# Optimization experiments

Hardware: AMD Instinct MI355X
Metric: run time of the kernel (lower is better)

## Reference

```python
import jax, jax.numpy as jnp
import numpy as np

B = 262144   # batch of candidate user-item pairs
D = 256      # concat embedding dim (embedding_dim*8)
H = 128      # hypernet hidden
HD = 32      # expert hidden dim
E = 4        # num experts


def setup_inputs() -> dict:
    key = jax.random.key(0)
    ks = jax.random.split(key, 16)
    def w(k, shape, fan_in):
        return jax.random.normal(k, shape, jnp.float32) * (1.0 / np.sqrt(fan_in))
    return {
        "x": jax.random.normal(ks[0], (B, D), jnp.float32),
        "context_embed": jax.random.normal(ks[1], (D,), jnp.float32),
        # hypernet (soft_module_route)
        "W1": w(ks[2], (D, H), D),   "b1": jnp.zeros((H,), jnp.float32),
        "W2": w(ks[3], (H, H), H),   "b2": jnp.zeros((H,), jnp.float32),
        "W12": w(ks[4], (H, E * E), H), "b12": jnp.zeros((E * E,), jnp.float32),
        "W22": w(ks[5], (H, E), H),     "b22": jnp.zeros((E,), jnp.float32),
        # soft_module experts: stacked per-expert Linear weights
        "Wf1": w(ks[6], (E, D, HD), D), "bf1": jnp.zeros((E, HD), jnp.float32),
        "Wf2": w(ks[7], (E, HD, HD), HD), "bf2": jnp.zeros((E, HD), jnp.float32),
        "Wfin": w(ks[8], (HD, 1), HD),  "bfin": jnp.zeros((1,), jnp.float32),
    }


def reference(x, context_embed, W1, b1, W2, b2, W12, b12, W22, b22,
              Wf1, bf1, Wf2, bf2, Wfin, bfin):
    # hypernet: routing weights from x * context
    embeds = x * context_embed[None, :]                       # [B,D]
    h = jax.nn.relu(embeds @ W1 + b1)                         # [B,H]
    c1 = jax.nn.softmax((h @ W12 + b12).reshape(-1, E, E), axis=1)   # [B,4,4]
    h2 = jax.nn.relu(h @ W2 + b2)                             # [B,H]
    c2 = jax.nn.softmax((h2 @ W22 + b22).reshape(-1, E, 1), axis=1)  # [B,4,1]
    # soft_module: 4 experts per layer, soft combined via c1/c2
    o1 = jax.nn.relu(jnp.einsum('bd,edh->bhe', x, Wf1) + bf1.T)      # [B,HD,E]
    in2 = jnp.einsum('bhe,bef->bhf', o1, c1)                         # [B,HD,E]
    o2 = jax.nn.relu(jnp.einsum('bhe,ehk->bke', in2, Wf2) + bf2.T)   # [B,HD,E]
    in3 = jnp.einsum('bke,bef->bkf', o2, c2)[..., 0]                 # [B,HD]
    return in3 @ Wfin + bfin                                         # [B,1]
```

## Files before the change

kernel.cpp:

```cpp
#include <hip/hip_runtime.h>
#include <hip/hip_bf16.h>

typedef _Float16 f16;
typedef _Float16 half8 __attribute__((ext_vector_type(8)));
typedef _Float16 half4 __attribute__((ext_vector_type(4)));
typedef float floatx4 __attribute__((ext_vector_type(4)));

#define BM 64

#define WA_OFF 0
#define WB_OFF 65536
#define WC_OFF 83968
#define WF2_OFF 86016
#define WSF_BYTE_OFF 180224
#define BA_OFF 0
#define BB_OFF 256
#define BCC_OFF 400
#define BF2_OFF 404
#define WFIN_OFF 532
#define BFIN_OFF 564

__global__ __launch_bounds__(256) void prep_kernel(
    const float* __restrict__ ctx, const float* __restrict__ W1,
    const float* __restrict__ b1, const float* __restrict__ W2,
    const float* __restrict__ b2, const float* __restrict__ W12,
    const float* __restrict__ b12, const float* __restrict__ W22,
    const float* __restrict__ b22, const float* __restrict__ Wf1,
    const float* __restrict__ bf1, const float* __restrict__ Wf2,
    const float* __restrict__ bf2, const float* __restrict__ Wfin,
    const float* __restrict__ bfin, f16* __restrict__ wsh,
    float* __restrict__ wsf)
{
  int tid = blockIdx.x * 256 + threadIdx.x;
  if (tid < 65536) {
    int j = tid & 7, l = (tid >> 3) & 63, kt = (tid >> 9) & 7, nt = tid >> 12;
    int k = kt * 32 + ((l >> 4) << 3) + j, n = nt * 16 + (l & 15);
    float v;
    if (n < 128) v = ctx[k] * W1[k * 128 + n];
    else { int c = n - 128; v = Wf1[((c >> 5) * 256 + k) * 32 + (c & 31)]; }
    wsh[tid] = (f16)v;
  } else if (tid < WB_OFF + 18432) {
    int o = tid - WB_OFF;
    int j = o & 7, l = (o >> 3) & 63, kt = (o >> 9) & 3, nt = o >> 11;
    int k = kt * 32 + ((l >> 4) << 3) + j, n = nt * 16 + (l & 15);
    float v = (n < 128) ? W2[k * 128 + n] : W12[k * 16 + (n - 128)];
    wsh[tid] = (f16)v;
  } else if (tid < WC_OFF + 2048) {
    int o = tid - WC_OFF;
    int j = o & 7, l = (o >> 3) & 63, kt = (o >> 9) & 3;
    int k = kt * 32 + ((l >> 4) << 3) + j, n = l & 15;
    float v = (n < 4) ? W22[k * 4 + n] : 0.f;
    wsh[tid] = (f16)v;
  } else if (tid < WF2_OFF + 4096) {
    int o = tid - WF2_OFF;
    int j = o & 7, l = (o >> 3) & 63, ent = o >> 9;
    int e = ent >> 1, nt = ent & 1;
    int k = ((l >> 4) << 3) + j, n = nt * 16 + (l & 15);
    wsh[tid] = (f16)Wf2[(e * 32 + k) * 32 + n];
  } else if (tid < 90112 + 565) {
    int o = tid - 90112;
    float v;
    if (o < 128) v = b1[o];
    else if (o < 256) v = bf1[o - 128];
    else if (o < 384) v = b2[o - 256];
    else if (o < 400) v = b12[o - 384];
    else if (o < 404) v = b22[o - 400];
    else if (o < 532) v = bf2[o - 404];
    else if (o < 564) v = Wfin[o - 532];
    else v = bfin[0];
    wsf[o] = v;
  }
}

#define MFMA16(A, Bv, C) __builtin_amdgcn_mfma_f32_16x16x32_f16(A, Bv, C, 0, 0, 0)

#define H2_OFF 32768
#define L1_OFF 49152
#define PART_OFF 49152
#define C2_OFF 51200

__global__ __launch_bounds__(512, 3) void fused_kernel(
    const float* __restrict__ x, const f16* __restrict__ wsh,
    const float* __restrict__ wsf, float* __restrict__ out)
{
  __shared__ __attribute__((aligned(16))) char lds[52224];
  const int t = threadIdx.x;
  const int lane = t & 63;
  const int w = t >> 6;
  const int l15 = lane & 15;
  const int l4 = lane >> 4;
  const int sw = (l15 & 7) << 4;
  const size_t base = (size_t)blockIdx.x * BM;

#pragma unroll
  for (int it = 0; it < 4; ++it) {
    int c = it * 512 + t;
    int r = c >> 5;
    int k0 = (c & 31) << 3;
    const float4* xv = (const float4*)(x + (base + (size_t)r) * 256 + k0);
    float4 a = xv[0], b = xv[1];
    half8 hv;
    hv[0] = (f16)a.x; hv[1] = (f16)a.y; hv[2] = (f16)a.z; hv[3] = (f16)a.w;
    hv[4] = (f16)b.x; hv[5] = (f16)b.y; hv[6] = (f16)b.z; hv[7] = (f16)b.w;
    *(half8*)(lds + ((r * 512 + k0 * 2) ^ ((r & 7) << 4))) = hv;
  }
  __syncthreads();

  {
    floatx4 acc[2][4];
#pragma unroll
    for (int q = 0; q < 2; ++q)
#pragma unroll
      for (int mt = 0; mt < 4; ++mt) acc[q][mt] = (floatx4){0.f, 0.f, 0.f, 0.f};
    for (int kt = 0; kt < 8; ++kt) {
      half8 Bx[4];
#pragma unroll
      for (int mt = 0; mt < 4; ++mt) {
        int r = mt * 16 + l15;
        Bx[mt] = *(const half8*)(lds + ((r * 512 + kt * 64 + (l4 << 4)) ^ sw));
      }
#pragma unroll
      for (int q = 0; q < 2; ++q) {
        half8 Wf = *(const half8*)(wsh + WA_OFF + (size_t)(((w * 2 + q) * 8 + kt) * 64 + lane) * 8);
#pragma unroll
        for (int mt = 0; mt < 4; ++mt) acc[q][mt] = MFMA16(Wf, Bx[mt], acc[q][mt]);
      }
    }
    __syncthreads();
#pragma unroll
    for (int q = 0; q < 2; ++q) {
      int c0 = (w * 2 + q) * 16 + l4 * 4;
      float4 bias = *(const float4*)(wsf + BA_OFF + c0);
#pragma unroll
      for (int mt = 0; mt < 4; ++mt) {
        int r = mt * 16 + l15;
        half4 hv;
#pragma unroll
        for (int i = 0; i < 4; ++i) hv[i] = (f16)fmaxf(acc[q][mt][i] + ((const float*)&bias)[i], 0.f);
        *(half4*)(lds + ((r * 512 + c0 * 2) ^ sw)) = hv;
      }
    }
  }
  __syncthreads();

  {
    floatx4 acc2[4];
    floatx4 accL[4];
#pragma unroll
    for (int mt = 0; mt < 4; ++mt) {
      acc2[mt] = (floatx4){0.f, 0.f, 0.f, 0.f};
      accL[mt] = (floatx4){0.f, 0.f, 0.f, 0.f};
    }
    for (int kt = 0; kt < 4; ++kt) {
      half8 Bh[4];
#pragma unroll
      for (int mt = 0; mt < 4; ++mt) {
        int r = mt * 16 + l15;
        Bh[mt] = *(const half8*)(lds + ((r * 512 + kt * 64 + (l4 << 4)) ^ sw));
      }
      half8 Wf = *(const half8*)(wsh + WB_OFF + (size_t)((w * 4 + kt) * 64 + lane) * 8);
#pragma unroll
      for (int mt = 0; mt < 4; ++mt) acc2[mt] = MFMA16(Wf, Bh[mt], acc2[mt]);
      if (w == 7) {
        half8 WfL = *(const half8*)(wsh + WB_OFF + (size_t)((32 + kt) * 64 + lane) * 8);
#pragma unroll
        for (int mt = 0; mt < 4; ++mt) accL[mt] = MFMA16(WfL, Bh[mt], accL[mt]);
      }
    }
    {
      int c0 = w * 16 + l4 * 4;
      float4 bias = *(const float4*)(wsf + BB_OFF + c0);
#pragma unroll
      for (int mt = 0; mt < 4; ++mt) {
        int r = mt * 16 + l15;
        half4 hv;
#pragma unroll
        for (int i = 0; i < 4; ++i) hv[i] = (f16)fmaxf(acc2[mt][i] + ((const float*)&bias)[i], 0.f);
        *(half4*)(lds + H2_OFF + ((r * 256 + c0 * 2) ^ ((r & 7) << 4))) = hv;
      }
    }
    if (w == 7) {
      float4 biasL = *(const float4*)(wsf + BB_OFF + 128 + l4 * 4);
#pragma unroll
      for (int mt = 0; mt < 4; ++mt) {
        int r = mt * 16 + l15;
        half4 hv;
#pragma unroll
        for (int i = 0; i < 4; ++i) hv[i] = (f16)(accL[mt][i] + ((const float*)&biasL)[i]);
        *(half4*)(lds + L1_OFF + r * 32 + l4 * 8) = hv;
      }
    }
  }
  __syncthreads();

  if (w < 4) {
    floatx4 acc3 = (floatx4){0.f, 0.f, 0.f, 0.f};
    int r3 = w * 16 + l15;
#pragma unroll
    for (int kt = 0; kt < 4; ++kt) {
      half8 Bh2 = *(const half8*)(lds + H2_OFF + ((r3 * 256 + kt * 64 + (l4 << 4)) ^ ((r3 & 7) << 4)));
      half8 Wf = *(const half8*)(wsh + WC_OFF + (size_t)(kt * 64 + lane) * 8);
      acc3 = MFMA16(Wf, Bh2, acc3);
    }
    if (lane < 16) {
      float4 bias = *(const float4*)(wsf + BCC_OFF);
      float q0 = acc3[0] + bias.x, q1 = acc3[1] + bias.y;
      float q2 = acc3[2] + bias.z, q3 = acc3[3] + bias.w;
      float m2 = fmaxf(fmaxf(q0, q1), fmaxf(q2, q3));
      float f0 = __expf(q0 - m2), f1 = __expf(q1 - m2);
      float f2 = __expf(q2 - m2), f3 = __expf(q3 - m2);
      float inv2 = 1.f / (f0 + f1 + f2 + f3);
      float4 c2o;
      c2o.x = f0 * inv2; c2o.y = f1 * inv2; c2o.z = f2 * inv2; c2o.w = f3 * inv2;
      *(float4*)(lds + C2_OFF + r3 * 16) = c2o;
    }
  }
  {
    int r = t >> 3, f = (t >> 1) & 3, hh = t & 1;
    const f16* L1p = (const f16*)(lds + L1_OFF) + r * 16 + f;
    float a0 = (float)L1p[0], a1 = (float)L1p[4], a2 = (float)L1p[8], a3 = (float)L1p[12];
    float m = fmaxf(fmaxf(a0, a1), fmaxf(a2, a3));
    float e0 = __expf(a0 - m), e1 = __expf(a1 - m), e2 = __expf(a2 - m), e3 = __expf(a3 - m);
    float inv = 1.f / (e0 + e1 + e2 + e3);
    f16 c0h = (f16)(e0 * inv), c1h = (f16)(e1 * inv);
    f16 c2h = (f16)(e2 * inv), c3h = (f16)(e3 * inv);
    int swr = (r & 7) << 4;
#pragma unroll
    for (int hi = 0; hi < 2; ++hi) {
      int h8 = hh * 2 + hi;
      half8 o0 = *(const half8*)(lds + ((r * 512 + 256 + 0   + h8 * 16) ^ swr));
      half8 o1v = *(const half8*)(lds + ((r * 512 + 256 + 64  + h8 * 16) ^ swr));
      half8 o2v = *(const half8*)(lds + ((r * 512 + 256 + 128 + h8 * 16) ^ swr));
      half8 o3v = *(const half8*)(lds + ((r * 512 + 256 + 192 + h8 * 16) ^ swr));
      half8 res = o0 * c0h + o1v * c1h + o2v * c2h + o3v * c3h;
      *(half8*)(lds + ((r * 512 + f * 64 + h8 * 16) ^ swr)) = res;
    }
  }
  __syncthreads();

  {
    int e = w & 3, ct = w >> 2;
    half8 Wfv = *(const half8*)(wsh + WF2_OFF + (size_t)((e * 2 + ct) * 64 + lane) * 8);
    float4 bv = *(const float4*)(wsf + BF2_OFF + e * 32 + ct * 16 + l4 * 4);
    float4 wfv = *(const float4*)(wsf + WFIN_OFF + ct * 16 + l4 * 4);
    floatx4 a4[4];
#pragma unroll
    for (int mt = 0; mt < 4; ++mt) a4[mt] = (floatx4){0.f, 0.f, 0.f, 0.f};
#pragma unroll
    for (int mt = 0; mt < 4; ++mt) {
      int r = mt * 16 + l15;
      half8 Bi = *(const half8*)(lds + ((r * 512 + e * 64 + (l4 << 4)) ^ ((r & 7) << 4)));
      a4[mt] = MFMA16(Wfv, Bi, a4[mt]);
    }
#pragma unroll
    for (int mt = 0; mt < 4; ++mt) {
      int r = mt * 16 + l15;
      float s = 0.f;
#pragma unroll
      for (int i = 0; i < 4; ++i)
        s += fmaxf(a4[mt][i] + ((const float*)&bv)[i], 0.f) * ((const float*)&wfv)[i];
      s += __shfl_xor(s, 16);
      s += __shfl_xor(s, 32);
      if (l4 == 0) {
        float c2e = *(const float*)(lds + C2_OFF + r * 16 + e * 4);
        *(float*)(lds + PART_OFF + r * 32 + w * 4) = s * c2e;
      }
    }
  }
  __syncthreads();

  if (t < 64) {
    float4 p0 = *(const float4*)(lds + PART_OFF + t * 32);
    float4 p1 = *(const float4*)(lds + PART_OFF + t * 32 + 16);
    out[base + t] = wsf[BFIN_OFF] + p0.x + p0.y + p0.z + p0.w + p1.x + p1.y + p1.z + p1.w;
  }
}

extern "C" void kernel_launch(void* const* d_in, const int* in_sizes, int n_in,
                              void* d_out, int out_size, void* d_ws, size_t ws_size,
                              hipStream_t stream) {
  (void)in_sizes; (void)n_in; (void)ws_size;
  const float* x    = (const float*)d_in[0];
  const float* ctx  = (const float*)d_in[1];
  const float* W1   = (const float*)d_in[2];
  const float* b1   = (const float*)d_in[3];
  const float* W2   = (const float*)d_in[4];
  const float* b2   = (const float*)d_in[5];
  const float* W12  = (const float*)d_in[6];
  const float* b12  = (const float*)d_in[7];
  const float* W22  = (const float*)d_in[8];
  const float* b22  = (const float*)d_in[9];
  const float* Wf1  = (const float*)d_in[10];
  const float* bf1  = (const float*)d_in[11];
  const float* Wf2  = (const float*)d_in[12];
  const float* bf2  = (const float*)d_in[13];
  const float* Wfin = (const float*)d_in[14];
  const float* bfin = (const float*)d_in[15];

  f16* wsh = (f16*)d_ws;
  float* wsf = (float*)((char*)d_ws + WSF_BYTE_OFF);

  prep_kernel<<<355, 256, 0, stream>>>(ctx, W1, b1, W2, b2, W12, b12, W22, b22,
                                       Wf1, bf1, Wf2, bf2, Wfin, bfin, wsh, wsf);

  int nblocks = 262144 / BM;
  fused_kernel<<<nblocks, 512, 0, stream>>>(x, wsh, wsf, (float*)d_out);
}
```

Measured before the change: 111.3 us.

## Make fused kernel persistent with register prefetch of next x tile

Launches a fixed grid of 768 blocks that loop over 64-row tiles instead of one block per tile. Each block loads the next tile's x rows into registers while the current tile's later stages run, overlapping global loads with compute. The 32 extra float registers per thread motivate lowering the launch-bounds occupancy hint from 3 to 2 blocks per CU, and the tile loop adds a loop-carried dependency with less block-level parallelism to hide latency.

```diff
diff --git a/kernel.cpp b/kernel.cpp
--- a/kernel.cpp
+++ b/kernel.cpp
@@ -7,6 +7,8 @@
 typedef float floatx4 __attribute__((ext_vector_type(4)));
 
 #define BM 64
+#define NBLK 768
+#define NTILE 4096
 
 #define WA_OFF 0
 #define WB_OFF 65536
@@ -79,7 +81,7 @@
 #define PART_OFF 49152
 #define C2_OFF 51200
 
-__global__ __launch_bounds__(512, 3) void fused_kernel(
+__global__ __launch_bounds__(512, 2) void fused_kernel(
     const float* __restrict__ x, const f16* __restrict__ wsh,
     const float* __restrict__ wsf, float* __restrict__ out)
 {
@@ -90,189 +92,225 @@
   const int l15 = lane & 15;
   const int l4 = lane >> 4;
   const int sw = (l15 & 7) << 4;
-  const size_t base = (size_t)blockIdx.x * BM;
-
-#pragma unroll
-  for (int it = 0; it < 4; ++it) {
-    int c = it * 512 + t;
-    int r = c >> 5;
-    int k0 = (c & 31) << 3;
-    const float4* xv = (const float4*)(x + (base + (size_t)r) * 256 + k0);
-    float4 a = xv[0], b = xv[1];
-    half8 hv;
-    hv[0] = (f16)a.x; hv[1] = (f16)a.y; hv[2] = (f16)a.z; hv[3] = (f16)a.w;
-    hv[4] = (f16)b.x; hv[5] = (f16)b.y; hv[6] = (f16)b.z; hv[7] = (f16)b.w;
-    *(half8*)(lds + ((r * 512 + k0 * 2) ^ ((r & 7) << 4))) = hv;
+
+  float4 nx[8];
+
+  int tile = blockIdx.x;
+  {
+    const float* xb = x + (size_t)tile * BM * 256;
+#pragma unroll
+    for (int it = 0; it < 4; ++it) {
+      int c = it * 512 + t;
+      int r = c >> 5;
+      int k0 = (c & 31) << 3;
+      const float4* xv = (const float4*)(xb + r * 256 + k0);
+      nx[it * 2] = xv[0];
+      nx[it * 2 + 1] = xv[1];
+    }
   }
-  __syncthreads();
-
-  {
-    floatx4 acc[2][4];
-#pragma unroll
-    for (int q = 0; q < 2; ++q)
-#pragma unroll
-      for (int mt = 0; mt < 4; ++mt) acc[q][mt] = (floatx4){0.f, 0.f, 0.f, 0.f};
-    for (int kt = 0; kt < 8; ++kt) {
-      half8 Bx[4];
+
+  while (true) {
+    const size_t base = (size_t)tile * BM;
+
+#pragma unroll
+    for (int it = 0; it < 4; ++it) {
+      int c = it * 512 + t;
+      int r = c >> 5;
+      int k0 = (c & 31) << 3;
+      float4 a = nx[it * 2], b = nx[it * 2 + 1];
+      half8 hv;
+      hv[0] = (f16)a.x; hv[1] = (f16)a.y; hv[2] = (f16)a.z; hv[3] = (f16)a.w;
+      hv[4] = (f16)b.x; hv[5] = (f16)b.y; hv[6] = (f16)b.z; hv[7] = (f16)b.w;
+      *(half8*)(lds + ((r * 512 + k0 * 2) ^ ((r & 7) << 4))) = hv;
+    }
+    __syncthreads();
+
+    {
+      floatx4 acc[2][4];
+#pragma unroll
+      for (int q = 0; q < 2; ++q)
+#pragma unroll
+        for (int mt = 0; mt < 4; ++mt) acc[q][mt] = (floatx4){0.f, 0.f, 0.f, 0.f};
+      for (int kt = 0; kt < 8; ++kt) {
+        half8 Bx[4];
+#pragma unroll
+        for (int mt = 0; mt < 4; ++mt) {
+          int r = mt * 16 + l15;
+          Bx[mt] = *(const half8*)(lds + ((r * 512 + kt * 64 + (l4 << 4)) ^ sw));
+        }
+#pragma unroll
+        for (int q = 0; q < 2; ++q) {
+          half8 Wf = *(const half8*)(wsh + WA_OFF + (size_t)(((w * 2 + q) * 8 + kt) * 64 + lane) * 8);
+#pragma unroll
+          for (int mt = 0; mt < 4; ++mt) acc[q][mt] = MFMA16(Wf, Bx[mt], acc[q][mt]);
+        }
+      }
+      __syncthreads();
+#pragma unroll
+      for (int q = 0; q < 2; ++q) {
+        int c0 = (w * 2 + q) * 16 + l4 * 4;
+        float4 bias = *(const float4*)(wsf + BA_OFF + c0);
+#pragma unroll
+        for (int mt = 0; mt < 4; ++mt) {
+          int r = mt * 16 + l15;
+          half4 hv;
+#pragma unroll
+          for (int i = 0; i < 4; ++i) hv[i] = (f16)fmaxf(acc[q][mt][i] + ((const float*)&bias)[i], 0.f);
+          *(half4*)(lds + ((r * 512 + c0 * 2) ^ sw)) = hv;
+        }
+      }
+    }
+
+    const int next = tile + NBLK;
+    const bool has_next = next < NTILE;
+    if (has_next) {
+      const float* xb = x + (size_t)next * BM * 256;
+#pragma unroll
+      for (int it = 0; it < 4; ++it) {
+        int c = it * 512 + t;
+        int r = c >> 5;
+        int k0 = (c & 31) << 3;
+        const float4* xv = (const float4*)(xb + r * 256 + k0);
+        nx[it * 2] = xv[0];
+        nx[it * 2 + 1] = xv[1];
+      }
+    }
+    __syncthreads();
+
+    {
+      floatx4 acc2[4];
+      floatx4 accL[4];
+#pragma unroll
+      for (int mt = 0; mt < 4; ++mt) {
+        acc2[mt] = (floatx4){0.f, 0.f, 0.f, 0.f};
+        accL[mt] = (floatx4){0.f, 0.f, 0.f, 0.f};
+      }
+      for (int kt = 0; kt < 4; ++kt) {
+        half8 Bh[4];
+#pragma unroll
+        for (int mt = 0; mt < 4; ++mt) {
+          int r = mt * 16 + l15;
+          Bh[mt] = *(const half8*)(lds + ((r * 512 + kt * 64 + (l4 << 4)) ^ sw));
+        }
+        half8 Wf = *(const half8*)(wsh + WB_OFF + (size_t)((w * 4 + kt) * 64 + lane) * 8);
+#pragma unroll
+        for (int mt = 0; mt < 4; ++mt) acc2[mt] = MFMA16(Wf, Bh[mt], acc2[mt]);
+        if (w == 7) {
+          half8 WfL = *(const half8*)(wsh + WB_OFF + (size_t)((32 + kt) * 64 + lane) * 8);
+#pragma unroll
+          for (int mt = 0; mt < 4; ++mt) accL[mt] = MFMA16(WfL, Bh[mt], accL[mt]);
+        }
+      }
+      {
+        int c0 = w * 16 + l4 * 4;
+        float4 bias = *(const float4*)(wsf + BB_OFF + c0);
+#pragma unroll
+        for (int mt = 0; mt < 4; ++mt) {
+          int r = mt * 16 + l15;
+          half4 hv;
+#pragma unroll
+          for (int i = 0; i < 4; ++i) hv[i] = (f16)fmaxf(acc2[mt][i] + ((const float*)&bias)[i], 0.f);
+          *(half4*)(lds + H2_OFF + ((r * 256 + c0 * 2) ^ ((r & 7) << 4))) = hv;
+        }
+      }
+      if (w == 7) {
+        float4 biasL = *(const float4*)(wsf + BB_OFF + 128 + l4 * 4);
+#pragma unroll
+        for (int mt = 0; mt < 4; ++mt) {
+          int r = mt * 16 + l15;
+          half4 hv;
+#pragma unroll
+          for (int i = 0; i < 4; ++i) hv[i] = (f16)(accL[mt][i] + ((const float*)&biasL)[i]);
+          *(half4*)(lds + L1_OFF + r * 32 + l4 * 8) = hv;
+        }
+      }
+    }
+    __syncthreads();
+
+    if (w < 4) {
+      floatx4 acc3 = (floatx4){0.f, 0.f, 0.f, 0.f};
+      int r3 = w * 16 + l15;
+#pragma unroll
+      for (int kt = 0; kt < 4; ++kt) {
+        half8 Bh2 = *(const half8*)(lds + H2_OFF + ((r3 * 256 + kt * 64 + (l4 << 4)) ^ ((r3 & 7) << 4)));
+        half8 Wf = *(const half8*)(wsh + WC_OFF + (size_t)(kt * 64 + lane) * 8);
+        acc3 = MFMA16(Wf, Bh2, acc3);
+      }
+      if (lane < 16) {
+        float4 bias = *(const float4*)(wsf + BCC_OFF);
+        float q0 = acc3[0] + bias.x, q1 = acc3[1] + bias.y;
+        float q2 = acc3[2] + bias.z, q3 = acc3[3] + bias.w;
+        float m2 = fmaxf(fmaxf(q0, q1), fmaxf(q2, q3));
+        float f0 = __expf(q0 - m2), f1 = __expf(q1 - m2);
+        float f2 = __expf(q2 - m2), f3 = __expf(q3 - m2);
+        float inv2 = 1.f / (f0 + f1 + f2 + f3);
+        float4 c2o;
+        c2o.x = f0 * inv2; c2o.y = f1 * inv2; c2o.z = f2 * inv2; c2o.w = f3 * inv2;
+        *(float4*)(lds + C2_OFF + r3 * 16) = c2o;
+      }
+    }
+    {
+      int r = t >> 3, f = (t >> 1) & 3, hh = t & 1;
+      const f16* L1p = (const f16*)(lds + L1_OFF) + r * 16 + f;
+      float a0 = (float)L1p[0], a1 = (float)L1p[4], a2 = (float)L1p[8], a3 = (float)L1p[12];
+      float m = fmaxf(fmaxf(a0, a1), fmaxf(a2, a3));
+      float e0 = __expf(a0 - m), e1 = __expf(a1 - m), e2 = __expf(a2 - m), e3 = __expf(a3 - m);
+      float inv = 1.f / (e0 + e1 + e2 + e3);
+      f16 c0h = (f16)(e0 * inv), c1h = (f16)(e1 * inv);
+      f16 c2h = (f16)(e2 * inv), c3h = (f16)(e3 * inv);
+      int swr = (r & 7) << 4;
+#pragma unroll
+      for (int hi = 0; hi < 2; ++hi) {
+        int h8 = hh * 2 + hi;
+        half8 o0 = *(const half8*)(lds + ((r * 512 + 256 + 0   + h8 * 16) ^ swr));
+        half8 o1v = *(const half8*)(lds + ((r * 512 + 256 + 64  + h8 * 16) ^ swr));
+        half8 o2v = *(const half8*)(lds + ((r * 512 + 256 + 128 + h8 * 16) ^ swr));
+        half8 o3v = *(const half8*)(lds + ((r * 512 + 256 + 192 + h8 * 16) ^ swr));
+        half8 res = o0 * c0h + o1v * c1h + o2v * c2h + o3v * c3h;
+        *(half8*)(lds + ((r * 512 + f * 64 + h8 * 16) ^ swr)) = res;
+      }
+    }
+    __syncthreads();
+
+    {
+      int e = w & 3, ct = w >> 2;
+      half8 Wfv = *(const half8*)(wsh + WF2_OFF + (size_t)((e * 2 + ct) * 64 + lane) * 8);
+      float4 bv = *(const float4*)(wsf + BF2_OFF + e * 32 + ct * 16 + l4 * 4);
+      float4 wfv = *(const float4*)(wsf + WFIN_OFF + ct * 16 + l4 * 4);
+      floatx4 a4[4];
+#pragma unroll
+      for (int mt = 0; mt < 4; ++mt) a4[mt] = (floatx4){0.f, 0.f, 0.f, 0.f};
 #pragma unroll
       for (int mt = 0; mt < 4; ++mt) {
         int r = mt * 16 + l15;
-        Bx[mt] = *(const half8*)(lds + ((r * 512 + kt * 64 + (l4 << 4)) ^ sw));
-      }
-#pragma unroll
-      for (int q = 0; q < 2; ++q) {
-        half8 Wf = *(const half8*)(wsh + WA_OFF + (size_t)(((w * 2 + q) * 8 + kt) * 64 + lane) * 8);
-#pragma unroll
-        for (int mt = 0; mt < 4; ++mt) acc[q][mt] = MFMA16(Wf, Bx[mt], acc[q][mt]);
-      }
-    }
-    __syncthreads();
-#pragma unroll
-    for (int q = 0; q < 2; ++q) {
-      int c0 = (w * 2 + q) * 16 + l4 * 4;
-      float4 bias = *(const float4*)(wsf + BA_OFF + c0);
+        half8 Bi = *(const half8*)(lds + ((r * 512 + e * 64 + (l4 << 4)) ^ ((r & 7) << 4)));
+        a4[mt] = MFMA16(Wfv, Bi, a4[mt]);
+      }
 #pragma unroll
       for (int mt = 0; mt < 4; ++mt) {
         int r = mt * 16 + l15;
-        half4 hv;
-#pragma unroll
-        for (int i = 0; i < 4; ++i) hv[i] = (f16)fmaxf(acc[q][mt][i] + ((const float*)&bias)[i], 0.f);
-        *(half4*)(lds + ((r * 512 + c0 * 2) ^ sw)) = hv;
-      }
-    }
-  }
-  __syncthreads();
-
-  {
-    floatx4 acc2[4];
-    floatx4 accL[4];
-#pragma unroll
-    for (int mt = 0; mt < 4; ++mt) {
-      acc2[mt] = (floatx4){0.f, 0.f, 0.f, 0.f};
-      accL[mt] = (floatx4){0.f, 0.f, 0.f, 0.f};
-    }
-    for (int kt = 0; kt < 4; ++kt) {
-      half8 Bh[4];
-#pragma unroll
-      for (int mt = 0; mt < 4; ++mt) {
-        int r = mt * 16 + l15;
-        Bh[mt] = *(const half8*)(lds + ((r * 512 + kt * 64 + (l4 << 4)) ^ sw));
-      }
-      half8 Wf = *(const half8*)(wsh + WB_OFF + (size_t)((w * 4 + kt) * 64 + lane) * 8);
-#pragma unroll
-      for (int mt = 0; mt < 4; ++mt) acc2[mt] = MFMA16(Wf, Bh[mt], acc2[mt]);
-      if (w == 7) {
-        half8 WfL = *(const half8*)(wsh + WB_OFF + (size_t)((32 + kt) * 64 + lane) * 8);
-#pragma unroll
-        for (int mt = 0; mt < 4; ++mt) accL[mt] = MFMA16(WfL, Bh[mt], accL[mt]);
-      }
-    }
-    {
-      int c0 = w * 16 + l4 * 4;
-      float4 bias = *(const float4*)(wsf + BB_OFF + c0);
-#pragma unroll
-      for (int mt = 0; mt < 4; ++mt) {
-        int r = mt * 16 + l15;
-        half4 hv;
-#pragma unroll
-        for (int i = 0; i < 4; ++i) hv[i] = (f16)fmaxf(acc2[mt][i] + ((const float*)&bias)[i], 0.f);
-        *(half4*)(lds + H2_OFF + ((r * 256 + c0 * 2) ^ ((r & 7) << 4))) = hv;
-      }
-    }
-    if (w == 7) {
-      float4 biasL = *(const float4*)(wsf + BB_OFF + 128 + l4 * 4);
-#pragma unroll
-      for (int mt = 0; mt < 4; ++mt) {
-        int r = mt * 16 + l15;
-        half4 hv;
-#pragma unroll
-        for (int i = 0; i < 4; ++i) hv[i] = (f16)(accL[mt][i] + ((const float*)&biasL)[i]);
-        *(half4*)(lds + L1_OFF + r * 32 + l4 * 8) = hv;
-      }
-    }
-  }
-  __syncthreads();
-
-  if (w < 4) {
-    floatx4 acc3 = (floatx4){0.f, 0.f, 0.f, 0.f};
-    int r3 = w * 16 + l15;
-#pragma unroll
-    for (int kt = 0; kt < 4; ++kt) {
-      half8 Bh2 = *(const half8*)(lds + H2_OFF + ((r3 * 256 + kt * 64 + (l4 << 4)) ^ ((r3 & 7) << 4)));
-      half8 Wf = *(const half8*)(wsh + WC_OFF + (size_t)(kt * 64 + lane) * 8);
-      acc3 = MFMA16(Wf, Bh2, acc3);
-    }
-    if (lane < 16) {
-      float4 bias = *(const float4*)(wsf + BCC_OFF);
-      float q0 = acc3[0] + bias.x, q1 = acc3[1] + bias.y;
-      float q2 = acc3[2] + bias.z, q3 = acc3[3] + bias.w;
-      float m2 = fmaxf(fmaxf(q0, q1), fmaxf(q2, q3));
-      float f0 = __expf(q0 - m2), f1 = __expf(q1 - m2);
-      float f2 = __expf(q2 - m2), f3 = __expf(q3 - m2);
-      float inv2 = 1.f / (f0 + f1 + f2 + f3);
-      float4 c2o;
-      c2o.x = f0 * inv2; c2o.y = f1 * inv2; c2o.z = f2 * inv2; c2o.w = f3 * inv2;
-      *(float4*)(lds + C2_OFF + r3 * 16) = c2o;
-    }
-  }
-  {
-    int r = t >> 3, f = (t >> 1) & 3, hh = t & 1;
-    const f16* L1p = (const f16*)(lds + L1_OFF) + r * 16 + f;
-    float a0 = (float)L1p[0], a1 = (float)L1p[4], a2 = (float)L1p[8], a3 = (float)L1p[12];
-    float m = fmaxf(fmaxf(a0, a1), fmaxf(a2, a3));
-    float e0 = __expf(a0 - m), e1 = __expf(a1 - m), e2 = __expf(a2 - m), e3 = __expf(a3 - m);
-    float inv = 1.f / (e0 + e1 + e2 + e3);
-    f16 c0h = (f16)(e0 * inv), c1h = (f16)(e1 * inv);
-    f16 c2h = (f16)(e2 * inv), c3h = (f16)(e3 * inv);
-    int swr = (r & 7) << 4;
-#pragma unroll
-    for (int hi = 0; hi < 2; ++hi) {
-      int h8 = hh * 2 + hi;
-      half8 o0 = *(const half8*)(lds + ((r * 512 + 256 + 0   + h8 * 16) ^ swr));
-      half8 o1v = *(const half8*)(lds + ((r * 512 + 256 + 64  + h8 * 16) ^ swr));
-      half8 o2v = *(const half8*)(lds + ((r * 512 + 256 + 128 + h8 * 16) ^ swr));
-      half8 o3v = *(const half8*)(lds + ((r * 512 + 256 + 192 + h8 * 16) ^ swr));
-      half8 res = o0 * c0h + o1v * c1h + o2v * c2h + o3v * c3h;
-      *(half8*)(lds + ((r * 512 + f * 64 + h8 * 16) ^ swr)) = res;
-    }
-  }
-  __syncthreads();
-
-  {
-    int e = w & 3, ct = w >> 2;
-    half8 Wfv = *(const half8*)(wsh + WF2_OFF + (size_t)((e * 2 + ct) * 64 + lane) * 8);
-    float4 bv = *(const float4*)(wsf + BF2_OFF + e * 32 + ct * 16 + l4 * 4);
-    float4 wfv = *(const float4*)(wsf + WFIN_OFF + ct * 16 + l4 * 4);
-    floatx4 a4[4];
-#pragma unroll
-    for (int mt = 0; mt < 4; ++mt) a4[mt] = (floatx4){0.f, 0.f, 0.f, 0.f};
-#pragma unroll
-    for (int mt = 0; mt < 4; ++mt) {
-      int r = mt * 16 + l15;
-      half8 Bi = *(const half8*)(lds + ((r * 512 + e * 64 + (l4 << 4)) ^ ((r & 7) << 4)));
-      a4[mt] = MFMA16(Wfv, Bi, a4[mt]);
-    }
-#pragma unroll
-    for (int mt = 0; mt < 4; ++mt) {
-      int r = mt * 16 + l15;
-      float s = 0.f;
-#pragma unroll
-      for (int i = 0; i < 4; ++i)
-        s += fmaxf(a4[mt][i] + ((const float*)&bv)[i], 0.f) * ((const float*)&wfv)[i];
-      s += __shfl_xor(s, 16);
-      s += __shfl_xor(s, 32);
-      if (l4 == 0) {
-        float c2e = *(const float*)(lds + C2_OFF + r * 16 + e * 4);
-        *(float*)(lds + PART_OFF + r * 32 + w * 4) = s * c2e;
-      }
-    }
-  }
-  __syncthreads();
-
-  if (t < 64) {
-    float4 p0 = *(const float4*)(lds + PART_OFF + t * 32);
-    float4 p1 = *(const float4*)(lds + PART_OFF + t * 32 + 16);
-    out[base + t] = wsf[BFIN_OFF] + p0.x + p0.y + p0.z + p0.w + p1.x + p1.y + p1.z + p1.w;
+        float s = 0.f;
+#pragma unroll
+        for (int i = 0; i < 4; ++i)
+          s += fmaxf(a4[mt][i] + ((const float*)&bv)[i], 0.f) * ((const float*)&wfv)[i];
+        s += __shfl_xor(s, 16);
+        s += __shfl_xor(s, 32);
+        if (l4 == 0) {
+          float c2e = *(const float*)(lds + C2_OFF + r * 16 + e * 4);
+          *(float*)(lds + PART_OFF + r * 32 + w * 4) = s * c2e;
+        }
+      }
+    }
+    __syncthreads();
+
+    if (t < 64) {
+      float4 p0 = *(const float4*)(lds + PART_OFF + t * 32);
+      float4 p1 = *(const float4*)(lds + PART_OFF + t * 32 + 16);
+      out[base + t] = wsf[BFIN_OFF] + p0.x + p0.y + p0.z + p0.w + p1.x + p1.y + p1.z + p1.w;
+    }
+
+    if (!has_next) break;
+    tile = next;
   }
 }
 
@@ -303,6 +341,5 @@
   prep_kernel<<<355, 256, 0, stream>>>(ctx, W1, b1, W2, b2, W12, b12, W22, b22,
                                        Wf1, bf1, Wf2, bf2, Wfin, bfin, wsh, wsf);
 
-  int nblocks = 262144 / BM;
-  fused_kernel<<<nblocks, 512, 0, stream>>>(x, wsh, wsf, (float*)d_out);
+  fused_kernel<<<NBLK, 512, 0, stream>>>(x, wsh, wsf, (float*)d_out);
 }
```

Result: slower. 181.8 us (+63.4%).

## Use 4-wave blocks with MFMA-fragment LDS layout and per-wave more tiles

Applied to the files above, without the earlier changes.

Halves the block to 256 threads (4 waves) so each wave computes twice as many output column tiles, reusing each loaded LDS B-fragment across more MFMAs. LDS activations are reorganised into a fragment-major swizzled layout (fragaddr) so MFMA operand reads are contiguous per lane, and the expert stage now has each wave handle one expert for both column tiles. This trades more accumulator registers and fewer waves per block (launch bounds 256,2) for less LDS traffic and simpler reductions.

```diff
diff --git a/kernel.cpp b/kernel.cpp
--- a/kernel.cpp
+++ b/kernel.cpp
@@ -74,12 +74,17 @@
 
 #define MFMA16(A, Bv, C) __builtin_amdgcn_mfma_f32_16x16x32_f16(A, Bv, C, 0, 0, 0)
 
+__device__ __forceinline__ int fragaddr(int frag, int lanep) {
+  return frag * 1024 + ((lanep * 16) ^ (((lanep >> 3) & 7) << 4) ^ ((frag & 7) << 4));
+}
+
+#define O1_OFF 16384
 #define H2_OFF 32768
 #define L1_OFF 49152
 #define PART_OFF 49152
 #define C2_OFF 51200
 
-__global__ __launch_bounds__(512, 3) void fused_kernel(
+__global__ __launch_bounds__(256, 2) void fused_kernel(
     const float* __restrict__ x, const f16* __restrict__ wsh,
     const float* __restrict__ wsf, float* __restrict__ out)
 {
@@ -89,12 +94,12 @@
   const int w = t >> 6;
   const int l15 = lane & 15;
   const int l4 = lane >> 4;
-  const int sw = (l15 & 7) << 4;
   const size_t base = (size_t)blockIdx.x * BM;
-
-#pragma unroll
-  for (int it = 0; it < 4; ++it) {
-    int c = it * 512 + t;
+  const floatx4 zero4 = {0.f, 0.f, 0.f, 0.f};
+
+#pragma unroll
+  for (int it = 0; it < 8; ++it) {
+    int c = it * 256 + t;
     int r = c >> 5;
     int k0 = (c & 31) << 3;
     const float4* xv = (const float4*)(x + (base + (size_t)r) * 256 + k0);
@@ -102,107 +107,116 @@
     half8 hv;
     hv[0] = (f16)a.x; hv[1] = (f16)a.y; hv[2] = (f16)a.z; hv[3] = (f16)a.w;
     hv[4] = (f16)b.x; hv[5] = (f16)b.y; hv[6] = (f16)b.z; hv[7] = (f16)b.w;
-    *(half8*)(lds + ((r * 512 + k0 * 2) ^ ((r & 7) << 4))) = hv;
-  }
-  __syncthreads();
-
-  {
-    floatx4 acc[2][4];
-#pragma unroll
-    for (int q = 0; q < 2; ++q)
-#pragma unroll
-      for (int mt = 0; mt < 4; ++mt) acc[q][mt] = (floatx4){0.f, 0.f, 0.f, 0.f};
+    int frag = (r >> 4) * 8 + (k0 >> 5);
+    int lanep = (r & 15) + (((k0 >> 3) & 3) << 4);
+    *(half8*)(lds + fragaddr(frag, lanep)) = hv;
+  }
+  __syncthreads();
+
+  {
+    floatx4 acc[4][4];
+#pragma unroll
+    for (int q = 0; q < 4; ++q)
+#pragma unroll
+      for (int mt = 0; mt < 4; ++mt) acc[q][mt] = zero4;
     for (int kt = 0; kt < 8; ++kt) {
       half8 Bx[4];
 #pragma unroll
+      for (int mt = 0; mt < 4; ++mt)
+        Bx[mt] = *(const half8*)(lds + fragaddr(mt * 8 + kt, lane));
+#pragma unroll
+      for (int q = 0; q < 4; ++q) {
+        half8 Wf = *(const half8*)(wsh + WA_OFF + (size_t)(((w * 4 + q) * 8 + kt) * 64 + lane) * 8);
+#pragma unroll
+        for (int mt = 0; mt < 4; ++mt) acc[q][mt] = MFMA16(Wf, Bx[mt], acc[q][mt]);
+      }
+    }
+    __syncthreads();
+#pragma unroll
+    for (int q = 0; q < 4; ++q) {
+      int n0 = (w * 4 + q) * 16;
+      int n = n0 + l4 * 4;
+      float4 bias = *(const float4*)(wsf + BA_OFF + n);
+      int j0 = (l4 * 4) & 7;
+      int v4 = (n >> 3) & 3;
+#pragma unroll
       for (int mt = 0; mt < 4; ++mt) {
-        int r = mt * 16 + l15;
-        Bx[mt] = *(const half8*)(lds + ((r * 512 + kt * 64 + (l4 << 4)) ^ sw));
-      }
-#pragma unroll
-      for (int q = 0; q < 2; ++q) {
-        half8 Wf = *(const half8*)(wsh + WA_OFF + (size_t)(((w * 2 + q) * 8 + kt) * 64 + lane) * 8);
-#pragma unroll
-        for (int mt = 0; mt < 4; ++mt) acc[q][mt] = MFMA16(Wf, Bx[mt], acc[q][mt]);
-      }
-    }
-    __syncthreads();
-#pragma unroll
-    for (int q = 0; q < 2; ++q) {
-      int c0 = (w * 2 + q) * 16 + l4 * 4;
-      float4 bias = *(const float4*)(wsf + BA_OFF + c0);
-#pragma unroll
-      for (int mt = 0; mt < 4; ++mt) {
-        int r = mt * 16 + l15;
         half4 hv;
 #pragma unroll
         for (int i = 0; i < 4; ++i) hv[i] = (f16)fmaxf(acc[q][mt][i] + ((const float*)&bias)[i], 0.f);
-        *(half4*)(lds + ((r * 512 + c0 * 2) ^ sw)) = hv;
-      }
-    }
-  }
-  __syncthreads();
-
-  {
-    floatx4 acc2[4];
+        int lanep = l15 + (v4 << 4);
+        int addr;
+        if (n0 < 128) addr = fragaddr(mt * 4 + (n0 >> 5), lanep);
+        else addr = O1_OFF + fragaddr(((n0 - 128) >> 5) * 4 + mt, lanep);
+        *(half4*)(lds + addr + j0 * 2) = hv;
+      }
+    }
+  }
+  __syncthreads();
+
+  {
+    floatx4 acc2[2][4];
     floatx4 accL[4];
 #pragma unroll
-    for (int mt = 0; mt < 4; ++mt) {
-      acc2[mt] = (floatx4){0.f, 0.f, 0.f, 0.f};
-      accL[mt] = (floatx4){0.f, 0.f, 0.f, 0.f};
-    }
+    for (int q = 0; q < 2; ++q)
+#pragma unroll
+      for (int mt = 0; mt < 4; ++mt) acc2[q][mt] = zero4;
+#pragma unroll
+    for (int mt = 0; mt < 4; ++mt) accL[mt] = zero4;
     for (int kt = 0; kt < 4; ++kt) {
       half8 Bh[4];
 #pragma unroll
+      for (int mt = 0; mt < 4; ++mt)
+        Bh[mt] = *(const half8*)(lds + fragaddr(mt * 4 + kt, lane));
+#pragma unroll
+      for (int q = 0; q < 2; ++q) {
+        half8 Wf = *(const half8*)(wsh + WB_OFF + (size_t)(((w * 2 + q) * 4 + kt) * 64 + lane) * 8);
+#pragma unroll
+        for (int mt = 0; mt < 4; ++mt) acc2[q][mt] = MFMA16(Wf, Bh[mt], acc2[q][mt]);
+      }
+      if (w == 3) {
+        half8 WfL = *(const half8*)(wsh + WB_OFF + (size_t)((32 + kt) * 64 + lane) * 8);
+#pragma unroll
+        for (int mt = 0; mt < 4; ++mt) accL[mt] = MFMA16(WfL, Bh[mt], accL[mt]);
+      }
+    }
+#pragma unroll
+    for (int q = 0; q < 2; ++q) {
+      int n0 = (w * 2 + q) * 16;
+      int n = n0 + l4 * 4;
+      float4 bias = *(const float4*)(wsf + BB_OFF + n);
+      int j0 = (l4 * 4) & 7;
+      int v4 = (n >> 3) & 3;
+#pragma unroll
       for (int mt = 0; mt < 4; ++mt) {
-        int r = mt * 16 + l15;
-        Bh[mt] = *(const half8*)(lds + ((r * 512 + kt * 64 + (l4 << 4)) ^ sw));
-      }
-      half8 Wf = *(const half8*)(wsh + WB_OFF + (size_t)((w * 4 + kt) * 64 + lane) * 8);
-#pragma unroll
-      for (int mt = 0; mt < 4; ++mt) acc2[mt] = MFMA16(Wf, Bh[mt], acc2[mt]);
-      if (w == 7) {
-        half8 WfL = *(const half8*)(wsh + WB_OFF + (size_t)((32 + kt) * 64 + lane) * 8);
-#pragma unroll
-        for (int mt = 0; mt < 4; ++mt) accL[mt] = MFMA16(WfL, Bh[mt], accL[mt]);
-      }
-    }
-    {
-      int c0 = w * 16 + l4 * 4;
-      float4 bias = *(const float4*)(wsf + BB_OFF + c0);
+        half4 hv;
+#pragma unroll
+        for (int i = 0; i < 4; ++i) hv[i] = (f16)fmaxf(acc2[q][mt][i] + ((const float*)&bias)[i], 0.f);
+        *(half4*)(lds + H2_OFF + fragaddr(mt * 4 + (n0 >> 5), l15 + (v4 << 4)) + j0 * 2) = hv;
+      }
+    }
+    if (w == 3) {
+      float4 biasL = *(const float4*)(wsf + BB_OFF + 128 + l4 * 4);
 #pragma unroll
       for (int mt = 0; mt < 4; ++mt) {
-        int r = mt * 16 + l15;
         half4 hv;
 #pragma unroll
-        for (int i = 0; i < 4; ++i) hv[i] = (f16)fmaxf(acc2[mt][i] + ((const float*)&bias)[i], 0.f);
-        *(half4*)(lds + H2_OFF + ((r * 256 + c0 * 2) ^ ((r & 7) << 4))) = hv;
-      }
-    }
-    if (w == 7) {
-      float4 biasL = *(const float4*)(wsf + BB_OFF + 128 + l4 * 4);
-#pragma unroll
-      for (int mt = 0; mt < 4; ++mt) {
-        int r = mt * 16 + l15;
-        half4 hv;
-#pragma unroll
         for (int i = 0; i < 4; ++i) hv[i] = (f16)(accL[mt][i] + ((const float*)&biasL)[i]);
-        *(half4*)(lds + L1_OFF + r * 32 + l4 * 8) = hv;
-      }
-    }
-  }
-  __syncthreads();
-
-  if (w < 4) {
-    floatx4 acc3 = (floatx4){0.f, 0.f, 0.f, 0.f};
-    int r3 = w * 16 + l15;
+        *(half4*)(lds + L1_OFF + (mt * 16 + l15) * 32 + l4 * 8) = hv;
+      }
+    }
+  }
+  __syncthreads();
+
+  {
+    floatx4 acc3 = zero4;
 #pragma unroll
     for (int kt = 0; kt < 4; ++kt) {
-      half8 Bh2 = *(const half8*)(lds + H2_OFF + ((r3 * 256 + kt * 64 + (l4 << 4)) ^ ((r3 & 7) << 4)));
+      half8 Bh2 = *(const half8*)(lds + H2_OFF + fragaddr(w * 4 + kt, lane));
       half8 Wf = *(const half8*)(wsh + WC_OFF + (size_t)(kt * 64 + lane) * 8);
       acc3 = MFMA16(Wf, Bh2, acc3);
     }
-    if (lane < 16) {
+    if (l4 == 0) {
       float4 bias = *(const float4*)(wsf + BCC_OFF);
       float q0 = acc3[0] + bias.x, q1 = acc3[1] + bias.y;
       float q2 = acc3[2] + bias.z, q3 = acc3[3] + bias.w;
@@ -212,11 +226,11 @@
       float inv2 = 1.f / (f0 + f1 + f2 + f3);
       float4 c2o;
       c2o.x = f0 * inv2; c2o.y = f1 * inv2; c2o.z = f2 * inv2; c2o.w = f3 * inv2;
-      *(float4*)(lds + C2_OFF + r3 * 16) = c2o;
-    }
-  }
-  {
-    int r = t >> 3, f = (t >> 1) & 3, hh = t & 1;
+      *(float4*)(lds + C2_OFF + (w * 16 + l15) * 16) = c2o;
+    }
+  }
+  {
+    int r = t >> 2, f = t & 3;
     const f16* L1p = (const f16*)(lds + L1_OFF) + r * 16 + f;
     float a0 = (float)L1p[0], a1 = (float)L1p[4], a2 = (float)L1p[8], a3 = (float)L1p[12];
     float m = fmaxf(fmaxf(a0, a1), fmaxf(a2, a3));
@@ -224,55 +238,62 @@
     float inv = 1.f / (e0 + e1 + e2 + e3);
     f16 c0h = (f16)(e0 * inv), c1h = (f16)(e1 * inv);
     f16 c2h = (f16)(e2 * inv), c3h = (f16)(e3 * inv);
-    int swr = (r & 7) << 4;
-#pragma unroll
-    for (int hi = 0; hi < 2; ++hi) {
-      int h8 = hh * 2 + hi;
-      half8 o0 = *(const half8*)(lds + ((r * 512 + 256 + 0   + h8 * 16) ^ swr));
-      half8 o1v = *(const half8*)(lds + ((r * 512 + 256 + 64  + h8 * 16) ^ swr));
-      half8 o2v = *(const half8*)(lds + ((r * 512 + 256 + 128 + h8 * 16) ^ swr));
-      half8 o3v = *(const half8*)(lds + ((r * 512 + 256 + 192 + h8 * 16) ^ swr));
+    int mt = r >> 4;
+    int r15 = r & 15;
+#pragma unroll
+    for (int h8 = 0; h8 < 4; ++h8) {
+      int lanep = r15 + (h8 << 4);
+      half8 o0 = *(const half8*)(lds + O1_OFF + fragaddr(0 * 4 + mt, lanep));
+      half8 o1v = *(const half8*)(lds + O1_OFF + fragaddr(1 * 4 + mt, lanep));
+      half8 o2v = *(const half8*)(lds + O1_OFF + fragaddr(2 * 4 + mt, lanep));
+      half8 o3v = *(const half8*)(lds + O1_OFF + fragaddr(3 * 4 + mt, lanep));
       half8 res = o0 * c0h + o1v * c1h + o2v * c2h + o3v * c3h;
-      *(half8*)(lds + ((r * 512 + f * 64 + h8 * 16) ^ swr)) = res;
-    }
-  }
-  __syncthreads();
-
-  {
-    int e = w & 3, ct = w >> 2;
-    half8 Wfv = *(const half8*)(wsh + WF2_OFF + (size_t)((e * 2 + ct) * 64 + lane) * 8);
-    float4 bv = *(const float4*)(wsf + BF2_OFF + e * 32 + ct * 16 + l4 * 4);
-    float4 wfv = *(const float4*)(wsf + WFIN_OFF + ct * 16 + l4 * 4);
-    floatx4 a4[4];
-#pragma unroll
-    for (int mt = 0; mt < 4; ++mt) a4[mt] = (floatx4){0.f, 0.f, 0.f, 0.f};
-#pragma unroll
-    for (int mt = 0; mt < 4; ++mt) {
-      int r = mt * 16 + l15;
-      half8 Bi = *(const half8*)(lds + ((r * 512 + e * 64 + (l4 << 4)) ^ ((r & 7) << 4)));
-      a4[mt] = MFMA16(Wfv, Bi, a4[mt]);
-    }
+      *(half8*)(lds + fragaddr(f * 4 + mt, lanep)) = res;
+    }
+  }
+  __syncthreads();
+
+  {
+    half8 Bi[4];
+#pragma unroll
+    for (int mt = 0; mt < 4; ++mt)
+      Bi[mt] = *(const half8*)(lds + fragaddr(w * 4 + mt, lane));
+    floatx4 acc4[2][4];
+#pragma unroll
+    for (int ct = 0; ct < 2; ++ct) {
+      half8 Wfv = *(const half8*)(wsh + WF2_OFF + (size_t)((w * 2 + ct) * 64 + lane) * 8);
+#pragma unroll
+      for (int mt = 0; mt < 4; ++mt) {
+        floatx4 z = zero4;
+        acc4[ct][mt] = MFMA16(Wfv, Bi[mt], z);
+      }
+    }
+    float4 b0 = *(const float4*)(wsf + BF2_OFF + w * 32 + l4 * 4);
+    float4 b1 = *(const float4*)(wsf + BF2_OFF + w * 32 + 16 + l4 * 4);
+    float4 wf0 = *(const float4*)(wsf + WFIN_OFF + l4 * 4);
+    float4 wf1 = *(const float4*)(wsf + WFIN_OFF + 16 + l4 * 4);
 #pragma unroll
     for (int mt = 0; mt < 4; ++mt) {
       int r = mt * 16 + l15;
       float s = 0.f;
 #pragma unroll
-      for (int i = 0; i < 4; ++i)
-        s += fmaxf(a4[mt][i] + ((const float*)&bv)[i], 0.f) * ((const float*)&wfv)[i];
+      for (int i = 0; i < 4; ++i) {
+        s += fmaxf(acc4[0][mt][i] + ((const float*)&b0)[i], 0.f) * ((const float*)&wf0)[i];
+        s += fmaxf(acc4[1][mt][i] + ((const float*)&b1)[i], 0.f) * ((const float*)&wf1)[i];
+      }
       s += __shfl_xor(s, 16);
       s += __shfl_xor(s, 32);
       if (l4 == 0) {
-        float c2e = *(const float*)(lds + C2_OFF + r * 16 + e * 4);
-        *(float*)(lds + PART_OFF + r * 32 + w * 4) = s * c2e;
+        float c2e = *(const float*)(lds + C2_OFF + r * 16 + w * 4);
+        *(float*)(lds + PART_OFF + r * 16 + w * 4) = s * c2e;
       }
     }
   }
   __syncthreads();
 
   if (t < 64) {
-    float4 p0 = *(const float4*)(lds + PART_OFF + t * 32);
-    float4 p1 = *(const float4*)(lds + PART_OFF + t * 32 + 16);
-    out[base + t] = wsf[BFIN_OFF] + p0.x + p0.y + p0.z + p0.w + p1.x + p1.y + p1.z + p1.w;
+    float4 p = *(const float4*)(lds + PART_OFF + t * 16);
+    out[base + t] = wsf[BFIN_OFF] + p.x + p.y + p.z + p.w;
   }
 }
 
@@ -304,5 +325,5 @@
                                        Wf1, bf1, Wf2, bf2, Wfin, bfin, wsh, wsf);
 
   int nblocks = 262144 / BM;
-  fused_kernel<<<nblocks, 512, 0, stream>>>(x, wsh, wsf, (float*)d_out);
+  fused_kernel<<<nblocks, 256, 0, stream>>>(x, wsh, wsf, (float*)d_out);
 }
```

After: 102.5 us. 7.9% less time.
